# Kernel tuning notes

Measured on AMD Instinct MI355X. Metric: run time of the kernel, lower is better.

The kernel has to match this reference:

```python
import jax, jax.numpy as jnp
import numpy as np

B, T, C = 4, 4096, 1024


def setup_inputs() -> dict:
    key = jax.random.key(0)
    k_x, k_f, k_g, k_p = jax.random.split(key, 4)
    scale = 1.0 / np.sqrt(C)  # keep gate pre-activations well-scaled
    return {
        "x": jax.random.normal(k_x, (B, T, C), dtype=jnp.float32),
        "W_f_x": jax.random.normal(k_f, (C, C), dtype=jnp.float32) * scale,
        "W_g_x": jax.random.normal(k_g, (C, C), dtype=jnp.float32) * scale,
        "W_proj": jax.random.normal(k_p, (C, C), dtype=jnp.float32) * scale,
    }


def _cfc_scan(a, b):
    """Solve h_t = a_t * h_{t-1} + b_t with h_{-1}=0 along axis 1 (T).

    Associative op on linear maps: (A_l,B_l) then (A_r,B_r) composes to
    (A_r*A_l, A_r*B_l + B_r). With h_init=0, h_t = B-component.
    """
    def op(l, r):
        al, bl = l
        ar, br = r
        return ar * al, ar * bl + br
    _, h = jax.lax.associative_scan(op, (a, b), axis=1)
    return h


def reference(x, W_f_x, W_g_x, W_proj):
    # Gates depend on x only (parallel mode). nn.Linear: x @ W.T
    f = jax.nn.sigmoid(jnp.einsum("btc,dc->btd", x, W_f_x))  # (B,T,C)
    g = jnp.tanh(jnp.einsum("btc,dc->btd", x, W_g_x))        # (B,T,C)
    h = _cfc_scan(f, (1.0 - f) * g)                           # (B,T,C)
    return jnp.einsum("btc,dc->btd", h, W_proj)               # c_proj
```

## Files before the change

### kernel.cpp

```cpp
#include <hip/hip_runtime.h>
#include <hip/hip_bf16.h>
#include <stdint.h>

#define TT 4096
#define BB 4
#define CC 1024
#define MM (BB * TT)
#define NCHUNK 64
#define CHUNK_T (TT / NCHUNK)
#define NCHAIN (BB * CC)

typedef float f32x4 __attribute__((ext_vector_type(4)));
typedef __bf16 bf16x8 __attribute__((ext_vector_type(8)));

__device__ __forceinline__ float b2f(ushort u) {
  union { float f; uint32_t v; } x; x.v = ((uint32_t)u) << 16; return x.f;
}
__device__ __forceinline__ ushort f2b(float f) {
  union { float f; uint32_t u; } x; x.f = f;
  uint32_t r = x.u + 0x7fffu + ((x.u >> 16) & 1u);
  return (ushort)(r >> 16);
}

__device__ __forceinline__ void async_copy16(const ushort* g, ushort* l) {
  __builtin_amdgcn_global_load_lds(
      (__attribute__((address_space(1))) void*)(g),
      (__attribute__((address_space(3))) void*)(l), 16, 0, 0);
}

__global__ __launch_bounds__(256) void cvt_all(const float* __restrict__ x,
                                               const float* __restrict__ wf,
                                               const float* __restrict__ wg,
                                               const float* __restrict__ wp,
                                               ushort* __restrict__ xb,
                                               ushort* __restrict__ wcat,
                                               ushort* __restrict__ wpb) {
  const int i = blockIdx.x * 256 + threadIdx.x;
  const float* s; ushort* d; int off;
  if (i < 4194304)            { s = x;  d = xb;              off = i; }
  else if (i < 4456448)       { s = wf; d = wcat;            off = i - 4194304; }
  else if (i < 4718592)       { s = wg; d = wcat + 1048576;  off = i - 4456448; }
  else                        { s = wp; d = wpb;             off = i - 4718592; }
  float4 v = ((const float4*)s)[off];
  ushort4 o;
  o.x = f2b(v.x); o.y = f2b(v.y); o.z = f2b(v.z); o.w = f2b(v.w);
  ((ushort4*)d)[off] = o;
}

template <int MODE>
__global__ __launch_bounds__(512, 2) void gemm_bt(const ushort* __restrict__ A,
                                                  const ushort* __restrict__ Bw,
                                                  float* __restrict__ outF,
                                                  ushort* __restrict__ outB, int N) {
  constexpr int K = CC;
  __shared__ __align__(16) ushort sA[4 * 256 * 32];
  __shared__ __align__(16) ushort sB[4 * 256 * 32];

  const int tid = threadIdx.x;
  const int lane = tid & 63;
  const int w = tid >> 6;
  const int wm = w >> 2;
  const int wn = w & 3;

  const int nbx = N >> 8;
  const int cpx = (int)gridDim.x >> 3;
  const int bid = blockIdx.x;
  const int wg = (bid & 7) * cpx + (bid >> 3);
  const long n0 = (long)(wg % nbx) << 8;
  const long m0 = (long)(wg / nbx) << 8;

  const int srow = lane >> 2;
  const int goct = (lane & 3) ^ ((lane >> 3) & 3);
  const ushort* gA0 = A + (m0 + w * 16 + srow) * K + goct * 8;
  const ushort* gB0 = Bw + (n0 + w * 16 + srow) * K + goct * 8;
  const ushort* gA1 = gA0 + 128 * (long)K;
  const ushort* gB1 = gB0 + 128 * (long)K;
  ushort* dA0 = &sA[w * 512 + lane * 8];
  ushort* dA1 = dA0 + 4096;
  ushort* dB0 = &sB[w * 512 + lane * 8];
  ushort* dB1 = dB0 + 4096;

  const int rlo = lane & 15;
  const int kq = lane >> 4;
  const int slot = kq ^ ((rlo >> 1) & 3);
  const ushort* rA = &sA[wm * 4096 + rlo * 32 + slot * 8];
  const ushort* rB = &sB[wn * 2048 + rlo * 32 + slot * 8];

  f32x4 acc[8][4];
#pragma unroll
  for (int i = 0; i < 8; ++i)
#pragma unroll
    for (int j = 0; j < 4; ++j) acc[i][j] = (f32x4){0.f, 0.f, 0.f, 0.f};

  auto stage = [&](int buf, int ts) {
    const int o = ts * 32;
    const int lo = buf * 8192;
    async_copy16(gA0 + o, dA0 + lo);
    async_copy16(gA1 + o, dA1 + lo);
    async_copy16(gB0 + o, dB0 + lo);
    async_copy16(gB1 + o, dB1 + lo);
  };

  auto body = [&](int buf, bool do_stage, int ts) {
    bf16x8 af[8], bfr[4];
    const int lo = buf * 8192;
#pragma unroll
    for (int i = 0; i < 8; ++i) af[i] = *(const bf16x8*)(rA + lo + i * 512);
#pragma unroll
    for (int j = 0; j < 4; ++j) bfr[j] = *(const bf16x8*)(rB + lo + j * 512);
    if (do_stage) stage((buf + 2) & 3, ts);
    __builtin_amdgcn_s_setprio(1);
#pragma unroll
    for (int i = 0; i < 8; ++i)
#pragma unroll
      for (int j = 0; j < 4; ++j)
        acc[i][j] = __builtin_amdgcn_mfma_f32_16x16x32_bf16(bfr[j], af[i], acc[i][j], 0, 0, 0);
    __builtin_amdgcn_s_setprio(0);
  };

  stage(0, 0);
  stage(1, 1);
  asm volatile("s_waitcnt vmcnt(4)" ::: "memory");
  __builtin_amdgcn_s_barrier();
  __builtin_amdgcn_sched_barrier(0);

  for (int t4 = 0; t4 < 7; ++t4) {
#pragma unroll
    for (int u = 0; u < 4; ++u) {
      body(u, true, t4 * 4 + u + 2);
      asm volatile("s_waitcnt vmcnt(4)" ::: "memory");
      __builtin_amdgcn_s_barrier();
      __builtin_amdgcn_sched_barrier(0);
    }
  }
  body(0, true, 30);
  asm volatile("s_waitcnt vmcnt(4)" ::: "memory");
  __builtin_amdgcn_s_barrier();
  __builtin_amdgcn_sched_barrier(0);
  body(1, true, 31);
  asm volatile("s_waitcnt vmcnt(4)" ::: "memory");
  __builtin_amdgcn_s_barrier();
  __builtin_amdgcn_sched_barrier(0);
  body(2, false, 0);
  asm volatile("s_waitcnt vmcnt(0)" ::: "memory");
  __builtin_amdgcn_s_barrier();
  __builtin_amdgcn_sched_barrier(0);
  body(3, false, 0);

  const int mloc = lane & 15;
  const int nq = (lane >> 4) * 4;
#pragma unroll
  for (int i = 0; i < 8; ++i) {
    const long m = m0 + wm * 128 + i * 16 + mloc;
#pragma unroll
    for (int j = 0; j < 4; ++j) {
      const long nb = n0 + wn * 64 + j * 16 + nq;
      const f32x4 v = acc[i][j];
      if (MODE == 0) {
        *(f32x4*)(outF + m * N + nb) = v;
      } else {
        float act[4];
        if (n0 < CC) {
#pragma unroll
          for (int r = 0; r < 4; ++r)
            act[r] = __builtin_amdgcn_rcpf(1.f + __expf(-v[r]));
        } else {
#pragma unroll
          for (int r = 0; r < 4; ++r)
            act[r] = fmaf(-2.f, __builtin_amdgcn_rcpf(1.f + __expf(2.f * v[r])), 1.f);
        }
        ushort4 o;
        o.x = f2b(act[0]); o.y = f2b(act[1]); o.z = f2b(act[2]); o.w = f2b(act[3]);
        *(ushort4*)(outB + m * (long)N + nb) = o;
      }
    }
  }
}

__global__ __launch_bounds__(256) void scan_pass1(const ushort* __restrict__ P,
                                                  float* __restrict__ cA,
                                                  float* __restrict__ cB) {
  const int pc = blockIdx.x * 256 + threadIdx.x;
  const int chunk = blockIdx.y;
  const int b = pc >> 8, c4 = (pc & 255) * 4;
  const ushort4* p =
      (const ushort4*)(P + (size_t)(b * TT + chunk * CHUNK_T) * (2 * CC) + c4);
  float A[4] = {1.f, 1.f, 1.f, 1.f};
  float h[4] = {0.f, 0.f, 0.f, 0.f};
#pragma unroll 4
  for (int i = 0; i < CHUNK_T; ++i) {
    const ushort4 fu = p[0];
    const ushort4 gu = p[CC / 4];
    p += 2 * CC / 4;
    const float f[4] = {b2f(fu.x), b2f(fu.y), b2f(fu.z), b2f(fu.w)};
    const float g[4] = {b2f(gu.x), b2f(gu.y), b2f(gu.z), b2f(gu.w)};
#pragma unroll
    for (int r = 0; r < 4; ++r) {
      A[r] *= f[r];
      h[r] = fmaf(f[r], h[r], (1.f - f[r]) * g[r]);
    }
  }
  const int ci = chunk * NCHAIN + b * CC + c4;
  *(f32x4*)(cA + ci) = (f32x4){A[0], A[1], A[2], A[3]};
  *(f32x4*)(cB + ci) = (f32x4){h[0], h[1], h[2], h[3]};
}

__global__ __launch_bounds__(256) void scan_pass2(const float* __restrict__ cA,
                                                  const float* __restrict__ cB,
                                                  float* __restrict__ hinit) {
  const int chain = blockIdx.x * 256 + threadIdx.x;
  float h = 0.f;
  for (int j = 0; j < NCHUNK; ++j) {
    hinit[j * NCHAIN + chain] = h;
    h = fmaf(cA[j * NCHAIN + chain], h, cB[j * NCHAIN + chain]);
  }
}

__global__ __launch_bounds__(256) void scan_pass3(const ushort* __restrict__ P,
                                                  const float* __restrict__ hinit,
                                                  ushort* __restrict__ H) {
  const int pc = blockIdx.x * 256 + threadIdx.x;
  const int chunk = blockIdx.y;
  const int b = pc >> 8, c4 = (pc & 255) * 4;
  f32x4 hv = *(const f32x4*)(hinit + chunk * NCHAIN + b * CC + c4);
  float h[4] = {hv[0], hv[1], hv[2], hv[3]};
  const ushort4* p =
      (const ushort4*)(P + (size_t)(b * TT + chunk * CHUNK_T) * (2 * CC) + c4);
  ushort4* hp = (ushort4*)(H + (size_t)(b * TT + chunk * CHUNK_T) * CC + c4);
#pragma unroll 4
  for (int i = 0; i < CHUNK_T; ++i) {
    const ushort4 fu = p[0];
    const ushort4 gu = p[CC / 4];
    p += 2 * CC / 4;
    const float f[4] = {b2f(fu.x), b2f(fu.y), b2f(fu.z), b2f(fu.w)};
    const float g[4] = {b2f(gu.x), b2f(gu.y), b2f(gu.z), b2f(gu.w)};
    ushort4 o;
#pragma unroll
    for (int r = 0; r < 4; ++r)
      h[r] = fmaf(f[r], h[r], (1.f - f[r]) * g[r]);
    o.x = f2b(h[0]); o.y = f2b(h[1]); o.z = f2b(h[2]); o.w = f2b(h[3]);
    *hp = o;
    hp += CC / 4;
  }
}

extern "C" void kernel_launch(void* const* d_in, const int* in_sizes, int n_in,
                              void* d_out, int out_size, void* d_ws, size_t ws_size,
                              hipStream_t stream) {
  const float* x  = (const float*)d_in[0];
  const float* Wf = (const float*)d_in[1];
  const float* Wg = (const float*)d_in[2];
  const float* Wp = (const float*)d_in[3];

  char* ws = (char*)d_ws;
  ushort* xb   = (ushort*)(ws);
  ushort* Hb   = xb;
  ushort* Wcat = (ushort*)(ws + 33554432);
  ushort* Wpb  = (ushort*)(ws + 33554432 + 4194304);
  ushort* P    = (ushort*)(ws + 33554432 + 4194304 + 2097152);
  char* tail   = ws + 33554432 + 4194304 + 2097152 + 67108864;
  float* cA    = (float*)(tail);
  float* cB    = (float*)(tail + 1048576);
  float* hinit = (float*)(tail + 2097152);
  (void)ws_size; (void)in_sizes; (void)n_in; (void)out_size;

  cvt_all<<<19456, 256, 0, stream>>>(x, Wf, Wg, Wp, xb, Wcat, Wpb);

  gemm_bt<1><<<512, 512, 0, stream>>>(xb, Wcat, nullptr, P, 2 * CC);

  dim3 gs(NCHAIN / 4 / 256, NCHUNK);
  scan_pass1<<<gs, 256, 0, stream>>>(P, cA, cB);
  scan_pass2<<<NCHAIN / 256, 256, 0, stream>>>(cA, cB, hinit);
  scan_pass3<<<gs, 256, 0, stream>>>(P, hinit, Hb);

  gemm_bt<0><<<256, 512, 0, stream>>>(Hb, Wpb, (float*)d_out, nullptr, CC);
}
```

Before: 278.4 us.

## Software-pipeline LDS fragment reads across barriers in GEMM and double scan chunks

The GEMM main loop is restructured so each tile is split into two MFMA halves. The next tile's A/B fragments are read from LDS right after the barrier, while the second half of the current tile's MFMAs is still issuing, which hides LDS read latency behind compute at the cost of extra fragment registers. Separately, the scan chunk count is doubled, giving more parallelism in the chunked scan passes but a larger carry array. The carry buffers are relocated into the dead Wcat workspace region to fit the larger size.

```diff
diff --git a/kernel.cpp b/kernel.cpp
--- a/kernel.cpp
+++ b/kernel.cpp
@@ -6,7 +6,7 @@
 #define BB 4
 #define CC 1024
 #define MM (BB * TT)
-#define NCHUNK 64
+#define NCHUNK 128
 #define CHUNK_T (TT / NCHUNK)
 #define NCHAIN (BB * CC)
 
@@ -47,6 +47,37 @@
   ((ushort4*)d)[off] = o;
 }
 
+
+#define RD_A(dst, slotoff, ih)                                          \
+  _Pragma("unroll") for (int i_ = 0; i_ < 4; ++i_)                      \
+      dst[i_] = *(const bf16x8*)(rA + (slotoff) + ((ih)*4 + i_) * 512);
+
+#define RD_B(dst, slotoff)                                              \
+  _Pragma("unroll") for (int j_ = 0; j_ < 4; ++j_)                      \
+      dst[j_] = *(const bf16x8*)(rB + (slotoff) + j_ * 512);
+
+#define MM_HALF(afb, bfb, ih)                                           \
+  __builtin_amdgcn_s_setprio(1);                                        \
+  _Pragma("unroll") for (int i_ = 0; i_ < 4; ++i_)                      \
+  _Pragma("unroll") for (int j_ = 0; j_ < 4; ++j_)                      \
+      acc[(ih)*4 + i_][j_] = __builtin_amdgcn_mfma_f32_16x16x32_bf16(   \
+          bfb[j_], afb[i_], acc[(ih)*4 + i_][j_], 0, 0, 0);             \
+  __builtin_amdgcn_s_setprio(0);
+
+#define CKPT(n)                                                         \
+  asm volatile("s_waitcnt vmcnt(" #n ")" ::: "memory");                 \
+  __builtin_amdgcn_s_barrier();                                         \
+  __builtin_amdgcn_sched_barrier(0);
+
+#define TILE_BODY(s, ns, ss, ts, bfrC, bfrN, DO_STAGE, CKN)             \
+  RD_A(afY, (s) * 8192, 1);                                             \
+  if (DO_STAGE) stage((ss), (ts));                                      \
+  MM_HALF(afX, bfrC, 0);                                                \
+  CKPT(CKN);                                                            \
+  RD_A(afX, (ns) * 8192, 0);                                            \
+  RD_B(bfrN, (ns) * 8192);                                              \
+  MM_HALF(afY, bfrC, 1);
+
 template <int MODE>
 __global__ __launch_bounds__(512, 2) void gemm_bt(const ushort* __restrict__ A,
                                                   const ushort* __restrict__ Bw,
@@ -101,51 +132,27 @@
     async_copy16(gB1 + o, dB1 + lo);
   };
 
-  auto body = [&](int buf, bool do_stage, int ts) {
-    bf16x8 af[8], bfr[4];
-    const int lo = buf * 8192;
-#pragma unroll
-    for (int i = 0; i < 8; ++i) af[i] = *(const bf16x8*)(rA + lo + i * 512);
-#pragma unroll
-    for (int j = 0; j < 4; ++j) bfr[j] = *(const bf16x8*)(rB + lo + j * 512);
-    if (do_stage) stage((buf + 2) & 3, ts);
-    __builtin_amdgcn_s_setprio(1);
-#pragma unroll
-    for (int i = 0; i < 8; ++i)
-#pragma unroll
-      for (int j = 0; j < 4; ++j)
-        acc[i][j] = __builtin_amdgcn_mfma_f32_16x16x32_bf16(bfr[j], af[i], acc[i][j], 0, 0, 0);
-    __builtin_amdgcn_s_setprio(0);
-  };
+  bf16x8 afX[4], afY[4], bfrP[4], bfrQ[4];
 
   stage(0, 0);
   stage(1, 1);
-  asm volatile("s_waitcnt vmcnt(4)" ::: "memory");
-  __builtin_amdgcn_s_barrier();
-  __builtin_amdgcn_sched_barrier(0);
+  CKPT(4);
+  RD_A(afX, 0, 0);
+  RD_B(bfrP, 0);
 
   for (int t4 = 0; t4 < 7; ++t4) {
-#pragma unroll
-    for (int u = 0; u < 4; ++u) {
-      body(u, true, t4 * 4 + u + 2);
-      asm volatile("s_waitcnt vmcnt(4)" ::: "memory");
-      __builtin_amdgcn_s_barrier();
-      __builtin_amdgcn_sched_barrier(0);
-    }
-  }
-  body(0, true, 30);
-  asm volatile("s_waitcnt vmcnt(4)" ::: "memory");
-  __builtin_amdgcn_s_barrier();
-  __builtin_amdgcn_sched_barrier(0);
-  body(1, true, 31);
-  asm volatile("s_waitcnt vmcnt(4)" ::: "memory");
-  __builtin_amdgcn_s_barrier();
-  __builtin_amdgcn_sched_barrier(0);
-  body(2, false, 0);
-  asm volatile("s_waitcnt vmcnt(0)" ::: "memory");
-  __builtin_amdgcn_s_barrier();
-  __builtin_amdgcn_sched_barrier(0);
-  body(3, false, 0);
+    const int tb = t4 * 4;
+    TILE_BODY(0, 1, 2, tb + 2, bfrP, bfrQ, true, 4);
+    TILE_BODY(1, 2, 3, tb + 3, bfrQ, bfrP, true, 4);
+    TILE_BODY(2, 3, 0, tb + 4, bfrP, bfrQ, true, 4);
+    TILE_BODY(3, 0, 1, tb + 5, bfrQ, bfrP, true, 4);
+  }
+  TILE_BODY(0, 1, 2, 30, bfrP, bfrQ, true, 4);
+  TILE_BODY(1, 2, 3, 31, bfrQ, bfrP, true, 4);
+  TILE_BODY(2, 3, 0, 0, bfrP, bfrQ, false, 0);
+  RD_A(afY, 3 * 8192, 1);
+  MM_HALF(afX, bfrQ, 0);
+  MM_HALF(afY, bfrQ, 1);
 
   const int mloc = lane & 15;
   const int nq = (lane >> 4) * 4;
@@ -259,9 +266,9 @@
   ushort* Wpb  = (ushort*)(ws + 33554432 + 4194304);
   ushort* P    = (ushort*)(ws + 33554432 + 4194304 + 2097152);
   char* tail   = ws + 33554432 + 4194304 + 2097152 + 67108864;
-  float* cA    = (float*)(tail);
-  float* cB    = (float*)(tail + 1048576);
-  float* hinit = (float*)(tail + 2097152);
+  float* cA    = (float*)Wcat;
+  float* cB    = (float*)(((char*)Wcat) + 2097152);
+  float* hinit = (float*)(tail);
   (void)ws_size; (void)in_sizes; (void)n_in; (void)out_size;
 
   cvt_all<<<19456, 256, 0, stream>>>(x, Wf, Wg, Wp, xb, Wcat, Wpb);
```

New measurement: 268.3 us. 3.6% less time.
